# Performance work log

Hardware: AMD Instinct MI355X
Metric: run time of the kernel (lower is better)

## Reference

```python
import jax, jax.numpy as jnp
import numpy as np

H = 1024      # lstm_hidden_size
LABELS = 122  # slot label size


def setup_inputs() -> dict:
    key = jax.random.key(0)
    ks = jax.random.split(key, 8)
    s_in = 1.0 / np.sqrt(5 * H)
    s_h = 1.0 / np.sqrt(H)
    return {
        "x": jax.random.normal(ks[0], (1, 512, 2 * H), jnp.float32),
        "hi": jax.random.normal(ks[1], (1, 512, 2 * H), jnp.float32),
        # LSTM params (PyTorch layout: gates ordered i, f, g, o)
        "W_ih": jax.random.uniform(ks[2], (4 * H, 5 * H), jnp.float32, -s_in, s_in),
        "W_hh": jax.random.uniform(ks[3], (4 * H, H), jnp.float32, -s_h, s_h),
        "b_ih": jax.random.uniform(ks[4], (4 * H,), jnp.float32, -s_h, s_h),
        "b_hh": jax.random.uniform(ks[5], (4 * H,), jnp.float32, -s_h, s_h),
        "W_fc": jax.random.uniform(ks[6], (LABELS, H), jnp.float32, -s_h, s_h),
        "b_fc": jax.random.uniform(ks[7], (LABELS,), jnp.float32, -s_h, s_h),
    }


def _decode(x, hi, W_ih, W_hh, b_ih, b_hh, W_fc, b_fc):
    # x, hi: [1, L, 2H] -> per-step encoder features [L, 4H] (batch fixed at 1)
    feats = jnp.concatenate([x, hi], axis=-1)[0]
    bias = b_ih + b_hh

    def step(carry, f_t):
        h, c, prev_out = carry
        z = jnp.concatenate([f_t, prev_out])              # [5H]: cat(x_t, hi_t, out_{t-1})
        gates = W_ih @ z + W_hh @ h + bias                # [4H]
        i, f, g, o = jnp.split(gates, 4)
        c_new = jax.nn.sigmoid(f) * c + jax.nn.sigmoid(i) * jnp.tanh(g)
        h_new = jax.nn.sigmoid(o) * jnp.tanh(c_new)
        return (h_new, c_new, h_new), h_new

    zero = jnp.zeros((H,), x.dtype)
    _, outs = jax.lax.scan(step, (zero, zero, zero), feats)  # outs: [L, H]
    res = outs @ W_fc.T + b_fc                               # [L, LABELS]
    return res[None]                                         # [1, L, LABELS]


def reference(x, hi, W_ih, W_hh, b_ih, b_hh, W_fc, b_fc):
    return _decode(x, hi, W_ih, W_hh, b_ih, b_hh, W_fc, b_fc)
```

## Files before the change

kernel.cpp:

```cpp
#include <hip/hip_runtime.h>
#include <hip/hip_fp16.h>
#include <math.h>

#define HD    1024
#define SEQL  512
#define NLAB  122
#define NWG   128
#define TPW   512
#define JPW   8

#define OFF_MSG   ((size_t)0)
#define OFF_HALL  ((size_t)16384)
#define OFF_GATES ((size_t)2113536)
#define OFF_WR    ((size_t)10502144)
#define OFF_W1H   ((size_t)27279360)
#define OFF_FH    ((size_t)60833792)
#define WS_NEED   ((size_t)65028096)

typedef unsigned long long u64;
typedef _Float16 v8h __attribute__((ext_vector_type(8)));
typedef float v4f __attribute__((ext_vector_type(4)));
typedef float v2f __attribute__((ext_vector_type(2)));
typedef unsigned int v4u __attribute__((ext_vector_type(4)));

__global__ __launch_bounds__(256) void prep_wr(const float* __restrict__ W_ih,
                                               const float* __restrict__ W_hh,
                                               float* __restrict__ W_r2) {
    int o = blockIdx.x * 256 + threadIdx.x;
    int g   = o >> 13;
    int i   = (o >> 9) & 15;
    int t   = o & 511;
    int row = t & 31;
    int kq  = t >> 5;
    int gate = row >> 3;
    int jj   = row & 7;
    int R = (gate << 10) + (g << 3) + jj;
    int k = (kq << 6) + (i << 2);
    float4 wa = *(const float4*)(W_ih + (size_t)R * 5120 + 4096 + k);
    float4 wb = *(const float4*)(W_hh + (size_t)R * 1024 + k);
    float4 out;
    out.x = wa.x + wb.x; out.y = wa.y + wb.y; out.z = wa.z + wb.z; out.w = wa.w + wb.w;
    *(float4*)(W_r2 + (size_t)o * 4) = out;
}

static __device__ __forceinline__ uint4 pack8(float4 f0, float4 f1) {
    __half2 p0 = __floats2half2_rn(f0.x, f0.y);
    __half2 p1 = __floats2half2_rn(f0.z, f0.w);
    __half2 p2 = __floats2half2_rn(f1.x, f1.y);
    __half2 p3 = __floats2half2_rn(f1.z, f1.w);
    uint4 o;
    o.x = *(unsigned*)&p0; o.y = *(unsigned*)&p1;
    o.z = *(unsigned*)&p2; o.w = *(unsigned*)&p3;
    return o;
}

__global__ __launch_bounds__(256) void prep_fh(const float* __restrict__ x,
                                               const float* __restrict__ hi,
                                               uint4* __restrict__ F_h) {
    int o = blockIdx.x * 256 + threadIdx.x;
    int t = o >> 9;
    int u = o & 511;
    const float* src = (u < 256) ? (x  + (size_t)t * 2048 + u * 8)
                                 : (hi + (size_t)t * 2048 + (u - 256) * 8);
    F_h[o] = pack8(*(const float4*)src, *(const float4*)(src + 4));
}

__global__ __launch_bounds__(256) void prep_w1h(const float* __restrict__ W_ih,
                                                uint4* __restrict__ W1h) {
    int o = blockIdx.x * 256 + threadIdx.x;
    int r = o >> 9;
    int u = o & 511;
    const float* src = W_ih + (size_t)r * 5120 + u * 8;
    W1h[o] = pack8(*(const float4*)src, *(const float4*)(src + 4));
}

__global__ __launch_bounds__(256) void gates_mfma(const uint4* __restrict__ F_u4,
                                                  const uint4* __restrict__ W_u4,
                                                  const float* __restrict__ b_ih,
                                                  const float* __restrict__ b_hh,
                                                  float* __restrict__ gates_x) {
    __shared__ uint4 AsB[1024];
    const _Float16* Ash = (const _Float16*)AsB;
    const _Float16* Bsh = Ash + 4096;
    const int tid  = threadIdx.x;
    const int wv   = tid >> 6;
    const int lane = tid & 63;
    const int wr   = wv & 1;
    const int wc   = wv >> 1;
    const int n0 = blockIdx.x * 128;
    const int t0 = blockIdx.y * 128;

    const int u0 = tid * 2, u1 = tid * 2 + 1;
    const uint4* aSrc0 = F_u4 + (size_t)(t0 + (u0 >> 2)) * 512 + (u0 & 3);
    const uint4* aSrc1 = F_u4 + (size_t)(t0 + (u1 >> 2)) * 512 + (u1 & 3);
    const uint4* bSrc0 = W_u4 + (size_t)(n0 + (u0 >> 2)) * 512 + (u0 & 3);
    const uint4* bSrc1 = W_u4 + (size_t)(n0 + (u1 >> 2)) * 512 + (u1 & 3);

    v4f acc[4][4];
    #pragma unroll
    for (int mi = 0; mi < 4; ++mi)
        #pragma unroll
        for (int ni = 0; ni < 4; ++ni)
            acc[mi][ni] = (v4f){0.f, 0.f, 0.f, 0.f};

    const int aoff = (wr * 64 + (lane & 15)) * 32 + (lane >> 4) * 8;
    const int boff = (wc * 64 + (lane & 15)) * 32 + (lane >> 4) * 8;

    for (int it = 0; it < 128; ++it) {
        uint4 a0 = aSrc0[it * 4], a1 = aSrc1[it * 4];
        uint4 b0 = bSrc0[it * 4], b1 = bSrc1[it * 4];
        __syncthreads();
        AsB[u0]       = a0; AsB[u1]       = a1;
        AsB[512 + u0] = b0; AsB[512 + u1] = b1;
        __syncthreads();
        v8h a8[4], b8[4];
        #pragma unroll
        for (int mi = 0; mi < 4; ++mi)
            a8[mi] = *(const v8h*)(Ash + aoff + mi * 16 * 32);
        #pragma unroll
        for (int ni = 0; ni < 4; ++ni)
            b8[ni] = *(const v8h*)(Bsh + boff + ni * 16 * 32);
        #pragma unroll
        for (int mi = 0; mi < 4; ++mi)
            #pragma unroll
            for (int ni = 0; ni < 4; ++ni)
                acc[mi][ni] = __builtin_amdgcn_mfma_f32_16x16x32_f16(
                                  a8[mi], b8[ni], acc[mi][ni], 0, 0, 0);
    }

    #pragma unroll
    for (int ni = 0; ni < 4; ++ni) {
        int r = n0 + wc * 64 + ni * 16 + (lane & 15);
        int sidx = ((r & 1023) >> 3) * 32 + (r >> 10) * 8 + (r & 7);
        float bias = b_ih[r] + b_hh[r];
        #pragma unroll
        for (int mi = 0; mi < 4; ++mi) {
            int tb = t0 + wr * 64 + mi * 16 + ((lane >> 4) << 2);
            #pragma unroll
            for (int reg = 0; reg < 4; ++reg)
                gates_x[(size_t)(tb + reg) * 4096 + sidx] = acc[mi][ni][reg] + bias;
        }
    }
}

__global__ __launch_bounds__(256) void gates_gemm_f32(const float* __restrict__ x,
                                                      const float* __restrict__ hi,
                                                      const float* __restrict__ W_ih,
                                                      const float* __restrict__ b_ih,
                                                      const float* __restrict__ b_hh,
                                                      float* __restrict__ gates_x) {
    __shared__ float As[16][68];
    __shared__ float Bs[16][68];
    const int tid = threadIdx.x;
    const int r0 = blockIdx.x * 64;
    const int t0 = blockIdx.y * 64;
    const int tx = tid & 15, ty = tid >> 4;
    const int l   = tid & 63;
    const int kq4 = tid >> 6;

    float acc[4][4] = {};
    for (int kb = 0; kb < 4096; kb += 16) {
        int k = kb + kq4 * 4;
        const float* asrc = (k < 2048) ? (x  + (size_t)(t0 + l) * 2048 + k)
                                       : (hi + (size_t)(t0 + l) * 2048 + (k - 2048));
        float4 a4 = *(const float4*)asrc;
        float4 b4 = *(const float4*)(W_ih + (size_t)(r0 + l) * 5120 + k);
        __syncthreads();
        As[kq4 * 4 + 0][l] = a4.x; As[kq4 * 4 + 1][l] = a4.y;
        As[kq4 * 4 + 2][l] = a4.z; As[kq4 * 4 + 3][l] = a4.w;
        Bs[kq4 * 4 + 0][l] = b4.x; Bs[kq4 * 4 + 1][l] = b4.y;
        Bs[kq4 * 4 + 2][l] = b4.z; Bs[kq4 * 4 + 3][l] = b4.w;
        __syncthreads();
        #pragma unroll
        for (int kk = 0; kk < 16; ++kk) {
            float4 av = *(const float4*)&As[kk][ty * 4];
            float4 bv = *(const float4*)&Bs[kk][tx * 4];
            float a_[4] = {av.x, av.y, av.z, av.w};
            float b_[4] = {bv.x, bv.y, bv.z, bv.w};
            #pragma unroll
            for (int i = 0; i < 4; ++i)
                #pragma unroll
                for (int j = 0; j < 4; ++j)
                    acc[i][j] += a_[i] * b_[j];
        }
    }
    int r = r0 + tx * 4;
    float bias[4];
    #pragma unroll
    for (int j = 0; j < 4; ++j) bias[j] = b_ih[r + j] + b_hh[r + j];
    int gate = r >> 10;
    int g    = (r & 1023) >> 3;
    int jj   = r & 7;
    int sidx = g * 32 + gate * 8 + jj;
    #pragma unroll
    for (int i = 0; i < 4; ++i) {
        float4 o;
        o.x = acc[i][0] + bias[0]; o.y = acc[i][1] + bias[1];
        o.z = acc[i][2] + bias[2]; o.w = acc[i][3] + bias[3];
        *(float4*)(gates_x + (size_t)(t0 + ty * 4 + i) * 4096 + sidx) = o;
    }
}

__global__ __launch_bounds__(512, 1) void lstm_rec(const float* __restrict__ gates_x,
                                                   const float* __restrict__ W_r2,
                                                   float* __restrict__ h_all,
                                                   u64* h_msg) {
    const int g   = blockIdx.x;
    const int tid = threadIdx.x;
    const int row = tid & 31;
    const int kq  = tid >> 5;
    __shared__ float  gxs[SEQL * 32];
    __shared__ float4 h_s4[256];
    __shared__ float  partial[8][36];
    float* h_sf = (float*)h_s4;

    float4 w[16];
    {
        const float4* Wp = (const float4*)W_r2 + (size_t)g * 8192;
        #pragma unroll
        for (int i = 0; i < 16; ++i)
            w[i] = Wp[i * TPW + tid];
    }

    {
        float4* gxs4 = (float4*)gxs;
        const float* gsrc = gates_x + (size_t)g * 32;
        #pragma unroll
        for (int k = 0; k < 8; ++k) {
            int o4 = tid + k * 512;
            int s  = o4 >> 3, c4 = o4 & 7;
            gxs4[o4] = *(const float4*)(gsrc + (size_t)s * 4096 + c4 * 4);
        }
    }
    __syncthreads();

    float c = 0.f;
    int budget = 4000000;

    for (int s = 0; s < SEQL; ++s) {
        float gx = 0.f;
        if (tid < 32) gx = gxs[s * 32 + tid];

        {
            const u64 addr = (u64)(h_msg + (size_t)(s & 1) * HD + tid * 2);
            const unsigned want = (unsigned)s;
            v4u ra, rb;
            for (;;) {
                asm volatile(
                    "global_load_dwordx4 %0, %2, off sc1\n\t"
                    "global_load_dwordx4 %1, %2, off sc1\n\t"
                    "s_waitcnt vmcnt(0)"
                    : "=&v"(ra), "=&v"(rb)
                    : "v"(addr)
                    : "memory");
                if (ra.y == want && ra.w == want) break;
                if (rb.y == want && rb.w == want) { ra = rb; break; }
                if (--budget < 0) { ra = rb; break; }
            }
            ((v2f*)h_sf)[tid] = (v2f){__uint_as_float(ra.x), __uint_as_float(ra.z)};
        }
        asm volatile("" ::: "memory");

        float a0 = 0.f, a1 = 0.f, a2 = 0.f, a3 = 0.f;
        #pragma unroll
        for (int i = 0; i < 16; ++i) {
            float4 h4 = h_s4[kq * 16 + i];
            a0 += w[i].x * h4.x;
            a1 += w[i].y * h4.y;
            a2 += w[i].z * h4.z;
            a3 += w[i].w * h4.w;
        }
        float p = (a0 + a1) + (a2 + a3);
        p += __shfl_xor(p, 32, 64);
        if ((tid & 32) == 0)
            partial[tid >> 6][row] = p;
        __syncthreads();

        if (tid < 32) {
            float sum = gx;
            #pragma unroll
            for (int q = 0; q < 8; ++q) sum += partial[q][tid];
            bool isg = ((tid >> 3) == 2);
            float e   = __expf(isg ? -2.f * sum : -sum);
            float act = isg ? (2.f / (1.f + e) - 1.f) : (1.f / (1.f + e));
            int jj = tid & 7;
            float sf = __shfl(act,  8 + jj, 64);
            float tg = __shfl(act, 16 + jj, 64);
            float so = __shfl(act, 24 + jj, 64);
            if (tid < 8) {
                float si = act;
                c = sf * c + si * tg;
                float th = 2.f / (1.f + __expf(-2.f * c)) - 1.f;
                float h = so * th;
                int j = g * JPW + tid;
                h_all[(size_t)s * HD + j] = h;
                u64 m = ((u64)(unsigned)(s + 1) << 32)
                      | (u64)__float_as_uint(h);
                __hip_atomic_store(h_msg + (size_t)((s + 1) & 1) * HD + j, m,
                                   __ATOMIC_RELAXED, __HIP_MEMORY_SCOPE_AGENT);
            }
        }
    }
}

__global__ __launch_bounds__(128) void fc_out(const float* __restrict__ h_all,
                                              const float* __restrict__ W_fc,
                                              const float* __restrict__ b_fc,
                                              float* __restrict__ out) {
    const int t = blockIdx.x;
    const int tid = threadIdx.x;
    __shared__ float4 h_s[256];
    const float4* hsrc = (const float4*)(h_all + (size_t)t * HD);
    h_s[tid] = hsrc[tid];
    h_s[tid + 128] = hsrc[tid + 128];
    __syncthreads();
    if (tid < NLAB) {
        float acc = b_fc[tid];
        const float4* wp = (const float4*)(W_fc + (size_t)tid * HD);
        #pragma unroll 8
        for (int k4 = 0; k4 < 256; ++k4) {
            float4 w = wp[k4];
            float4 h = h_s[k4];
            acc += w.x*h.x + w.y*h.y + w.z*h.z + w.w*h.w;
        }
        out[(size_t)t * NLAB + tid] = acc;
    }
}

extern "C" void kernel_launch(void* const* d_in, const int* in_sizes, int n_in,
                              void* d_out, int out_size, void* d_ws, size_t ws_size,
                              hipStream_t stream) {
    const float* x    = (const float*)d_in[0];
    const float* hi   = (const float*)d_in[1];
    const float* W_ih = (const float*)d_in[2];
    const float* W_hh = (const float*)d_in[3];
    const float* b_ih = (const float*)d_in[4];
    const float* b_hh = (const float*)d_in[5];
    const float* W_fc = (const float*)d_in[6];
    const float* b_fc = (const float*)d_in[7];
    float* out = (float*)d_out;

    char* ws = (char*)d_ws;
    u64*   h_msg   = (u64*)(ws + OFF_MSG);
    float* h_all   = (float*)(ws + OFF_HALL);
    float* gates_x = (float*)(ws + OFF_GATES);
    float* W_r2    = (float*)(ws + OFF_WR);
    uint4* W1h     = (uint4*)(ws + OFF_W1H);
    uint4* F_h     = (uint4*)(ws + OFF_FH);

    hipMemsetAsync(d_ws, 0, 16384, stream);

    prep_wr<<<4096, 256, 0, stream>>>(W_ih, W_hh, W_r2);

    if (ws_size >= WS_NEED) {
        prep_fh<<<1024, 256, 0, stream>>>(x, hi, F_h);
        prep_w1h<<<8192, 256, 0, stream>>>(W_ih, W1h);
        dim3 gg(32, 4);
        gates_mfma<<<gg, 256, 0, stream>>>(F_h, W1h, b_ih, b_hh, gates_x);
    } else {
        dim3 gg(64, 8);
        gates_gemm_f32<<<gg, 256, 0, stream>>>(x, hi, W_ih, b_ih, b_hh, gates_x);
    }

    lstm_rec<<<NWG, TPW, 0, stream>>>(gates_x, W_r2, h_all, h_msg);

    fc_out<<<SEQL, 128, 0, stream>>>(h_all, W_fc, b_fc, out);
}
```

Measured before the change: 1.193 ms.

## Move recurrent weights to LDS and stream gate inputs from global per step

The per-workgroup recurrent weight slice now lives in LDS instead of 64 VGPRs per thread, and is reloaded into registers every timestep. The preloaded per-step input gate table is dropped from LDS and read from global memory each step. The spin-wait on the cross-workgroup h message now issues one load per poll instead of two and backs off with s_sleep after repeated misses. This trades register pressure and polling traffic for extra LDS reads and a global load on the serial critical path each step.

```diff
diff --git a/kernel.cpp b/kernel.cpp
--- a/kernel.cpp
+++ b/kernel.cpp
@@ -209,28 +209,16 @@
     const int tid = threadIdx.x;
     const int row = tid & 31;
     const int kq  = tid >> 5;
-    __shared__ float  gxs[SEQL * 32];
+    __shared__ float4 W_lds[16][TPW];
     __shared__ float4 h_s4[256];
     __shared__ float  partial[8][36];
     float* h_sf = (float*)h_s4;
 
-    float4 w[16];
     {
         const float4* Wp = (const float4*)W_r2 + (size_t)g * 8192;
         #pragma unroll
         for (int i = 0; i < 16; ++i)
-            w[i] = Wp[i * TPW + tid];
-    }
-
-    {
-        float4* gxs4 = (float4*)gxs;
-        const float* gsrc = gates_x + (size_t)g * 32;
-        #pragma unroll
-        for (int k = 0; k < 8; ++k) {
-            int o4 = tid + k * 512;
-            int s  = o4 >> 3, c4 = o4 & 7;
-            gxs4[o4] = *(const float4*)(gsrc + (size_t)s * 4096 + c4 * 4);
-        }
+            W_lds[i][tid] = Wp[i * TPW + tid];
     }
     __syncthreads();
 
@@ -239,23 +227,31 @@
 
     for (int s = 0; s < SEQL; ++s) {
         float gx = 0.f;
-        if (tid < 32) gx = gxs[s * 32 + tid];
+        if (tid < 32)
+            gx = gates_x[(size_t)s * 4096 + g * 32 + tid];
+
+        asm volatile("" ::: "memory");
+        float4 w[16];
+        #pragma unroll
+        for (int i = 0; i < 16; ++i)
+            w[i] = W_lds[i][tid];
+        asm volatile("" ::: "memory");
 
         {
             const u64 addr = (u64)(h_msg + (size_t)(s & 1) * HD + tid * 2);
             const unsigned want = (unsigned)s;
-            v4u ra, rb;
+            v4u ra;
+            int miss = 0;
             for (;;) {
                 asm volatile(
-                    "global_load_dwordx4 %0, %2, off sc1\n\t"
-                    "global_load_dwordx4 %1, %2, off sc1\n\t"
+                    "global_load_dwordx4 %0, %1, off sc1\n\t"
                     "s_waitcnt vmcnt(0)"
-                    : "=&v"(ra), "=&v"(rb)
+                    : "=&v"(ra)
                     : "v"(addr)
                     : "memory");
                 if (ra.y == want && ra.w == want) break;
-                if (rb.y == want && rb.w == want) { ra = rb; break; }
-                if (--budget < 0) { ra = rb; break; }
+                if (--budget < 0) break;
+                if (miss++) __builtin_amdgcn_s_sleep(2);
             }
             ((v2f*)h_sf)[tid] = (v2f){__uint_as_float(ra.x), __uint_as_float(ra.z)};
         }
```

Measured after the change: 1.156 ms. -3.1%, faster.
